# Optimization experiments

Measured on AMD Instinct MI355X. Metric: run time of the kernel, lower is better.

Reference implementation:

```python
import jax, jax.numpy as jnp
import numpy as np

C = 512
G = 32  # num_norm_groups
EPS = 1e-6


def setup_inputs() -> dict:
    key = jax.random.key(0)
    ks = jax.random.split(key, 10)
    B, H, W = 8, 64, 64
    s = 1.0 / np.sqrt(C)
    return {
        "x": jax.random.normal(ks[0], (B, C, H, W), dtype=jnp.float32),
        "gamma": jnp.ones((C,), jnp.float32),
        "beta": jnp.zeros((C,), jnp.float32),
        "Wq": jax.random.uniform(ks[1], (C, C), jnp.float32, -s, s),
        "bq": jax.random.uniform(ks[2], (C,), jnp.float32, -s, s),
        "Wk": jax.random.uniform(ks[3], (C, C), jnp.float32, -s, s),
        "bk": jax.random.uniform(ks[4], (C,), jnp.float32, -s, s),
        "Wv": jax.random.uniform(ks[5], (C, C), jnp.float32, -s, s),
        "bv": jax.random.uniform(ks[6], (C,), jnp.float32, -s, s),
        "Wo": jax.random.uniform(ks[7], (C, C), jnp.float32, -s, s),
    }


def group_norm(x, gamma, beta):
    # x: [B, C, H, W]; normalize over each group of C//G channels and all spatial dims
    B, Cc, H, W = x.shape
    xg = x.reshape(B, G, Cc // G, H, W)
    mean = jnp.mean(xg, axis=(2, 3, 4), keepdims=True)
    var = jnp.var(xg, axis=(2, 3, 4), keepdims=True)
    xg = (xg - mean) * jax.lax.rsqrt(var + EPS)
    x = xg.reshape(B, Cc, H, W)
    return x * gamma[None, :, None, None] + beta[None, :, None, None]


def reference(x, gamma, beta, Wq, bq, Wk, bk, Wv, bv, Wo):
    B, Cc, H, W = x.shape
    out = group_norm(x, gamma, beta)
    # [B, C, H, W] -> [B, H*W, C]
    out = out.transpose(0, 2, 3, 1).reshape(B, H * W, Cc)
    q = out @ Wq.T + bq
    k = out @ Wk.T + bk
    v = out @ Wv.T + bv
    score = jnp.einsum('bic,bjc->bij', q, k) / jnp.sqrt(jnp.float32(Cc))
    score = jax.nn.softmax(score, axis=-1)
    out = jnp.einsum('bij,bjc->bic', score, v)
    out = out @ Wo.T
    out = out.reshape(B, H, W, Cc).transpose(0, 3, 1, 2)
    return out + x
```

## Files before the change

kernel.cpp:

```cpp
#include <hip/hip_runtime.h>
#include <hip/hip_bf16.h>
#include <cstdint>
#include <cstddef>

typedef __hip_bfloat16 BF;
typedef __attribute__((ext_vector_type(8))) short bhalf8;
typedef __attribute__((ext_vector_type(4))) float floatx4;

#define NB 8
#define NC 512
#define NHW 4096
#define NG 32

__device__ __forceinline__ float b2f(short h) {
    union { unsigned u; float f; } c;
    c.u = ((unsigned)(unsigned short)h) << 16;
    return c.f;
}
__device__ __forceinline__ short f2b(float f) {
    __hip_bfloat16 h = __float2bfloat16(f);
    short s;
    __builtin_memcpy(&s, &h, 2);
    return s;
}

__device__ __forceinline__ void gload16(const BF* g, BF* l) {
    __builtin_amdgcn_global_load_lds(
        (const __attribute__((address_space(1))) void*)g,
        (__attribute__((address_space(3))) void*)l, 16, 0, 0);
}

__device__ __forceinline__ void BARRIER() {
    asm volatile("" ::: "memory");
    __builtin_amdgcn_s_barrier();
    asm volatile("" ::: "memory");
}
#define WAITVM(N) asm volatile("s_waitcnt vmcnt(" #N ")" ::: "memory")
#define WAITLGKM0() asm volatile("s_waitcnt lgkmcnt(0)" ::: "memory")
#define SB0() __builtin_amdgcn_sched_barrier(0)

#define DSR(dst, base, IMM) \
    asm volatile("ds_read_b128 %0, %1 offset:" #IMM : "=&v"(dst) : "v"(base))

__device__ __forceinline__ void xcd_swizzle(int& bx, int& by) {
    const int gx = gridDim.x;
    const int nwg = gx * gridDim.y;
    if ((nwg & 7) == 0) {
        const int lin = by * gx + bx;
        const int cpx = nwg >> 3;
        const int s = (lin & 7) * cpx + (lin >> 3);
        bx = s % gx;
        by = s / gx;
    }
}

struct QKVPtrs {
    BF* q; BF* k; BF* v;
    const float* bq; const float* bk; const float* bv;
};

__global__ __launch_bounds__(256) void f2b_convert4(const float* __restrict__ s0,
                                                    const float* __restrict__ s1,
                                                    const float* __restrict__ s2,
                                                    const float* __restrict__ s3,
                                                    BF* __restrict__ dst) {
    const int which = blockIdx.x >> 8;
    const float* src = (which == 0) ? s0 : (which == 1) ? s1 : (which == 2) ? s2 : s3;
    BF* d = dst + (long)which * (NC * NC);
    const int i = ((blockIdx.x & 255) * 256 + threadIdx.x) * 4;
    float4 v = *(const float4*)&src[i];
    d[i]     = __float2bfloat16(v.x);
    d[i + 1] = __float2bfloat16(v.y);
    d[i + 2] = __float2bfloat16(v.z);
    d[i + 3] = __float2bfloat16(v.w);
}

__global__ __launch_bounds__(256) void gn_stats_part(const float* __restrict__ x,
                                                     float2* __restrict__ part) {
    const int bg = blockIdx.x, qi = blockIdx.y;
    const long base = (long)bg * 65536 + (long)qi * 16384;
    float s = 0.f, q = 0.f;
    for (int i = threadIdx.x * 4; i < 16384; i += 256 * 4) {
        float4 v4 = *(const float4*)&x[base + i];
        s += v4.x + v4.y + v4.z + v4.w;
        q += v4.x * v4.x + v4.y * v4.y + v4.z * v4.z + v4.w * v4.w;
    }
#pragma unroll
    for (int o = 32; o; o >>= 1) { s += __shfl_down(s, o); q += __shfl_down(q, o); }
    __shared__ float rs[4], rq[4];
    const int w = threadIdx.x >> 6;
    if ((threadIdx.x & 63) == 0) { rs[w] = s; rq[w] = q; }
    __syncthreads();
    if (threadIdx.x == 0) {
        s = rs[0] + rs[1] + rs[2] + rs[3];
        q = rq[0] + rq[1] + rq[2] + rq[3];
        part[bg * 4 + qi] = make_float2(s, q);
    }
}

__global__ __launch_bounds__(256) void gn_finalize(const float2* __restrict__ part,
                                                   float* __restrict__ stats) {
    const int bg = threadIdx.x;
    float s = 0.f, q = 0.f;
#pragma unroll
    for (int j = 0; j < 4; j++) {
        float2 p = part[bg * 4 + j];
        s += p.x; q += p.y;
    }
    float mean = s * (1.f / 65536.f);
    float var = q * (1.f / 65536.f) - mean * mean;
    stats[2 * bg]     = mean;
    stats[2 * bg + 1] = rsqrtf(fmaxf(var, 0.f) + 1e-6f);
}

__global__ __launch_bounds__(256) void gn_apply(const float* __restrict__ x,
                                                const float* __restrict__ gamma,
                                                const float* __restrict__ beta,
                                                const float* __restrict__ stats,
                                                BF* __restrict__ n) {
    __shared__ float tile[64][65];
    const int b = blockIdx.z, c0 = blockIdx.y * 64, s0 = blockIdx.x * 64;
    const long xbase = ((long)b * NC + c0) * NHW + s0;
#pragma unroll
    for (int i = 0; i < 16; i++) {
        int lin = i * 256 + threadIdx.x;
        int cl = lin >> 6, sl = lin & 63;
        int c = c0 + cl;
        float2 mr = ((const float2*)stats)[b * NG + (c >> 4)];
        float v = x[xbase + (long)cl * NHW + sl];
        v = (v - mr.x) * mr.y * gamma[c] + beta[c];
        tile[cl][sl] = v;
    }
    __syncthreads();
    const long nbase = ((long)b * NHW + s0) * NC + c0;
#pragma unroll
    for (int i = 0; i < 16; i++) {
        int lin = i * 256 + threadIdx.x;
        int sl = lin >> 6, cl = lin & 63;
        n[nbase + (long)sl * NC + cl] = __float2bfloat16(tile[cl][sl]);
    }
}

#define RD_A_LO(b0, b1) { DSR(aR[0][0],b0,0);    DSR(aR[1][0],b0,2048); \
                          DSR(aR[2][0],b0,4096); DSR(aR[3][0],b0,6144); \
                          DSR(aR[0][1],b1,0);    DSR(aR[1][1],b1,2048); \
                          DSR(aR[2][1],b1,4096); DSR(aR[3][1],b1,6144); }
#define RD_A_HI(b0, b1) { DSR(aR[0][0],b0,8192);  DSR(aR[1][0],b0,10240); \
                          DSR(aR[2][0],b0,12288); DSR(aR[3][0],b0,14336); \
                          DSR(aR[0][1],b1,8192);  DSR(aR[1][1],b1,10240); \
                          DSR(aR[2][1],b1,12288); DSR(aR[3][1],b1,14336); }
#define RD_B_LO(b0, b1) { DSR(bR[0][0],b0,0);    DSR(bR[1][0],b0,2048); \
                          DSR(bR[0][1],b1,0);    DSR(bR[1][1],b1,2048); }
#define RD_B_HI(b0, b1) { DSR(bR[2][0],b0,4096); DSR(bR[3][0],b0,6144); \
                          DSR(bR[2][1],b1,4096); DSR(bR[3][1],b1,6144); }
#define QUAD(M0, N0)                                                                     \
    {                                                                                    \
        _Pragma("unroll") for (int ks = 0; ks < 2; ks++)                                 \
            _Pragma("unroll") for (int mf = (M0); mf < (M0) + 4; mf++)                   \
                _Pragma("unroll") for (int nf = (N0); nf < (N0) + 2; nf++)               \
                    acc[mf][nf] = __builtin_amdgcn_mfma_f32_16x16x32_bf16(               \
                        aR[mf & 3][ks], bR[nf][ks], acc[mf][nf], 0, 0, 0);               \
    }

template <bool BIAS, bool TRANS, bool RESID, bool QKV>
__global__ __launch_bounds__(512) void gemm256(
    const BF* __restrict__ A, long aStride,
    const BF* __restrict__ Bm, long bStride,
    BF* __restrict__ C, long cStride,
    const float* __restrict__ bias,
    const float* __restrict__ resid, float* __restrict__ outF,
    int M, int N, int K, float scale, long lda, long ldb, QKVPtrs P)
{
    __shared__ __align__(16) char sL[131072];
    const int tid = threadIdx.x;
    const int wave = tid >> 6, lane = tid & 63;
    int bxi = blockIdx.x, byi = blockIdx.y;
    xcd_swizzle(bxi, byi);
    const int bm = byi * 256, bn = bxi * 256;
    const int zz = blockIdx.z;
    const BF* Ab = A + (long)zz * aStride + (long)bm * lda;
    const BF* Bb = Bm + (long)zz * bStride + (long)bn * ldb;

    const int d0 = tid * 16, d1 = 8192 + tid * 16;
    const int r0 = d0 >> 7, r1 = d1 >> 7;
    const int c0s = ((d0 ^ ((r0 & 7) << 4)) & 127) >> 1;
    const int c1s = ((d1 ^ ((r1 & 7) << 4)) & 127) >> 1;
    const long sA0 = (long)r0 * lda + c0s, sA1 = (long)r1 * lda + c1s;
    const long sB0 = (long)r0 * ldb + c0s, sB1 = (long)r1 * ldb + c1s;
    const int lds0 = wave * 1024;
    const int lds1 = 8192 + wave * 1024;

    const int lr = lane & 15, lk2 = (lane >> 4) * 16;
    const int swz = (lr & 7) << 4;
    const int sb0 = lr * 128 + (lk2 ^ swz);
    const int sb1 = lr * 128 + ((lk2 + 64) ^ swz);
    const int aReg = (wave >> 2) * 16384;
    const int bReg = (2 + ((wave >> 1) & 1)) * 16384 + (wave & 1) * 8192;
    const int aI0 = aReg + sb0, aI1 = aReg + sb1;
    const int bI0 = bReg + sb0, bI1 = bReg + sb1;
    const int aJ0 = aI0 + 65536, aJ1 = aI1 + 65536;
    const int bJ0 = bI0 + 65536, bJ1 = bI1 + 65536;

    auto STAGE = [&](int t, int region, int dbuf) {
        const bool isA = region < 2;
        const long ld = isA ? lda : ldb;
        const BF* g = (isA ? (Ab + (long)region * 128 * ld)
                           : (Bb + (long)(region - 2) * 128 * ld)) + (long)t * 64;
        char* lb = sL + dbuf * 65536 + region * 16384;
        gload16(g + (isA ? sA0 : sB0), (BF*)(lb + lds0));
        gload16(g + (isA ? sA1 : sB1), (BF*)(lb + lds1));
    };

    floatx4 acc[8][4];
#pragma unroll
    for (int i = 0; i < 8; i++)
#pragma unroll
        for (int j = 0; j < 4; j++) acc[i][j] = (floatx4){0.f, 0.f, 0.f, 0.f};

    const int nt = K >> 6, ngrp = nt >> 1;

    STAGE(0, 0, 0); STAGE(0, 1, 0); STAGE(0, 2, 0); STAGE(0, 3, 0);
    WAITVM(4);
    STAGE(1, 2, 1); STAGE(1, 3, 1); STAGE(1, 0, 1);
    WAITVM(6);
    BARRIER();

    bhalf8 aR[4][2], bR[4][2];

    for (int g = 0; g < ngrp; ++g) {
        const bool st = (g < ngrp - 1);
        const int t2 = 2 * g + 2, t3 = 2 * g + 3;

        RD_A_LO(aI0, aI1);
        RD_B_LO(bI0, bI1);
        if (!(wave & 2)) { RD_B_HI(bI0, bI1); }
        STAGE(2 * g + 1, 1, 1);
        BARRIER(); WAITLGKM0(); SB0();
        __builtin_amdgcn_s_setprio(1);
        QUAD(0, 0);
        __builtin_amdgcn_s_setprio(0);
        BARRIER();

        if (wave & 2) { RD_B_HI(bI0, bI1); }
        if (st) STAGE(t2, 2, 0);
        BARRIER(); WAITLGKM0(); SB0();
        __builtin_amdgcn_s_setprio(1);
        QUAD(0, 2);
        __builtin_amdgcn_s_setprio(0);
        BARRIER();

        RD_A_HI(aI0, aI1);
        if (st) STAGE(t2, 3, 0);
        BARRIER(); WAITLGKM0(); SB0();
        __builtin_amdgcn_s_setprio(1);
        QUAD(4, 0);
        __builtin_amdgcn_s_setprio(0);
        BARRIER();

        if (st) STAGE(t2, 0, 0);
        BARRIER(); SB0();
        __builtin_amdgcn_s_setprio(1);
        QUAD(4, 2);
        __builtin_amdgcn_s_setprio(0);
        if (st) { WAITVM(6); } else { WAITVM(0); }
        BARRIER();

        RD_A_LO(aJ0, aJ1);
        RD_B_LO(bJ0, bJ1);
        if (!(wave & 2)) { RD_B_HI(bJ0, bJ1); }
        if (st) STAGE(t2, 1, 0);
        BARRIER(); WAITLGKM0(); SB0();
        __builtin_amdgcn_s_setprio(1);
        QUAD(0, 0);
        __builtin_amdgcn_s_setprio(0);
        BARRIER();

        if (wave & 2) { RD_B_HI(bJ0, bJ1); }
        if (st) STAGE(t3, 2, 1);
        BARRIER(); WAITLGKM0(); SB0();
        __builtin_amdgcn_s_setprio(1);
        QUAD(0, 2);
        __builtin_amdgcn_s_setprio(0);
        BARRIER();

        RD_A_HI(aJ0, aJ1);
        if (st) STAGE(t3, 3, 1);
        BARRIER(); WAITLGKM0(); SB0();
        __builtin_amdgcn_s_setprio(1);
        QUAD(4, 0);
        __builtin_amdgcn_s_setprio(0);
        BARRIER();

        if (st) STAGE(t3, 0, 1);
        BARRIER(); SB0();
        __builtin_amdgcn_s_setprio(1);
        QUAD(4, 2);
        __builtin_amdgcn_s_setprio(0);
        if (st) { WAITVM(6); }
        BARRIER();
    }

    const int wm = (wave >> 2) * 128, wn = (wave & 3) * 64;
    if (QKV) {
        const int sec = bn >> 9;
        const int cb = bn & 511;
        BF* Cb = (sec == 0 ? P.q : sec == 1 ? P.k : P.v) + (long)zz * cStride;
        const float* bb = (sec == 0 ? P.bq : sec == 1 ? P.bk : P.bv);
#pragma unroll
        for (int nf = 0; nf < 4; nf++) {
            const int col = cb + wn + nf * 16 + lr;
            const float bvv = bb[col];
#pragma unroll
            for (int mf = 0; mf < 8; mf++) {
                const int row0 = bm + wm + mf * 16 + (lane >> 4) * 4;
#pragma unroll
                for (int r = 0; r < 4; r++) {
                    float v = acc[mf][nf][r] * scale + bvv;
                    if (sec == 2) Cb[(long)col * M + row0 + r] = __float2bfloat16(v);
                    else          Cb[(long)(row0 + r) * NC + col] = __float2bfloat16(v);
                }
            }
        }
        return;
    }
    if (RESID) {
        float* Ob = outF + (long)zz * cStride;
        const float* Xb = resid + (long)zz * cStride;
#pragma unroll
        for (int nf = 0; nf < 4; nf++) {
            const int col = bn + wn + nf * 16 + lr;
#pragma unroll
            for (int mf = 0; mf < 8; mf++) {
                const int row0 = bm + wm + mf * 16 + (lane >> 4) * 4;
                const long a = (long)col * M + row0;
                float4 xv = *(const float4*)&Xb[a];
                float4 ov;
                ov.x = acc[mf][nf][0] * scale + xv.x;
                ov.y = acc[mf][nf][1] * scale + xv.y;
                ov.z = acc[mf][nf][2] * scale + xv.z;
                ov.w = acc[mf][nf][3] * scale + xv.w;
                *(float4*)&Ob[a] = ov;
            }
        }
        return;
    }
    BF* Cb = C + (long)zz * cStride;
#pragma unroll
    for (int nf = 0; nf < 4; nf++) {
        const int col = bn + wn + nf * 16 + lr;
        const float bv = BIAS ? bias[col] : 0.0f;
#pragma unroll
        for (int mf = 0; mf < 8; mf++) {
            const int row0 = bm + wm + mf * 16 + (lane >> 4) * 4;
#pragma unroll
            for (int r = 0; r < 4; r++) {
                float v = acc[mf][nf][r] * scale + bv;
                if (TRANS) Cb[(long)col * M + row0 + r] = __float2bfloat16(v);
                else       Cb[(long)(row0 + r) * N + col] = __float2bfloat16(v);
            }
        }
    }
}

template <bool BIAS, bool TRANS>
__global__ __launch_bounds__(256, 2) void gemm128(
    const BF* __restrict__ A, long aStride,
    const BF* __restrict__ Bm, long bStride,
    BF* __restrict__ C, long cStride,
    const float* __restrict__ bias,
    int M, int N, int K, float scale)
{
    __shared__ __align__(16) BF sA[128 * 32];
    __shared__ __align__(16) BF sB[128 * 32];
    const int tid = threadIdx.x;
    const int wave = tid >> 6, lane = tid & 63;
    int bxi = blockIdx.x, byi = blockIdx.y;
    xcd_swizzle(bxi, byi);
    const int bm = byi * 128, bn = bxi * 128;
    const BF* Ab = A + (long)blockIdx.z * aStride + (long)bm * K;
    const BF* Bb = Bm + (long)blockIdx.z * bStride + (long)bn * K;

    const int srow = wave * 32 + (lane >> 2);
    const int sk = (lane & 3) * 8;
    const BF* gA0 = Ab + (long)srow * K + sk;
    const BF* gA1 = gA0 + (long)16 * K;
    const BF* gB0 = Bb + (long)srow * K + sk;
    const BF* gB1 = gB0 + (long)16 * K;
    BF* lA0 = &sA[(wave * 32) * 32];
    BF* lA1 = &sA[(wave * 32 + 16) * 32];
    BF* lB0 = &sB[(wave * 32) * 32];
    BF* lB1 = &sB[(wave * 32 + 16) * 32];

    floatx4 acc[4][4];
#pragma unroll
    for (int i = 0; i < 4; i++)
#pragma unroll
        for (int j = 0; j < 4; j++) acc[i][j] = (floatx4){0.f, 0.f, 0.f, 0.f};

    const int wm = (wave >> 1) * 64, wn = (wave & 1) * 64;
    const int lr = lane & 15, lk = (lane >> 4) * 8;

    for (int k0 = 0; k0 < K; k0 += 32) {
        __syncthreads();
        gload16(gA0 + k0, lA0);
        gload16(gA1 + k0, lA1);
        gload16(gB0 + k0, lB0);
        gload16(gB1 + k0, lB1);
        __syncthreads();
        bhalf8 af[4], bfr[4];
#pragma unroll
        for (int i = 0; i < 4; i++)
            af[i] = *(const bhalf8*)&sA[(wm + i * 16 + lr) * 32 + lk];
#pragma unroll
        for (int i = 0; i < 4; i++)
            bfr[i] = *(const bhalf8*)&sB[(wn + i * 16 + lr) * 32 + lk];
#pragma unroll
        for (int mi = 0; mi < 4; mi++)
#pragma unroll
            for (int ni = 0; ni < 4; ni++)
                acc[mi][ni] = __builtin_amdgcn_mfma_f32_16x16x32_bf16(
                    af[mi], bfr[ni], acc[mi][ni], 0, 0, 0);
    }

    BF* Cb = C + (long)blockIdx.z * cStride;
#pragma unroll
    for (int ni = 0; ni < 4; ni++) {
        const int col = bn + wn + ni * 16 + lr;
        const float bv = BIAS ? bias[col] : 0.0f;
#pragma unroll
        for (int mi = 0; mi < 4; mi++) {
            const int row0 = bm + wm + mi * 16 + (lane >> 4) * 4;
#pragma unroll
            for (int r = 0; r < 4; r++) {
                float v = acc[mi][ni][r] * scale + bv;
                if (TRANS) Cb[(long)col * M + row0 + r] = __float2bfloat16(v);
                else       Cb[(long)(row0 + r) * N + col] = __float2bfloat16(v);
            }
        }
    }
}

__global__ __launch_bounds__(256, 2) void gemm64(
    const BF* __restrict__ A, long aStride,
    const BF* __restrict__ Bm, long bStride,
    BF* __restrict__ C, long cStride,
    int N, int K, float scale)
{
    __shared__ __align__(16) BF sA[64 * 32];
    __shared__ __align__(16) BF sB[128 * 32];
    const int tid = threadIdx.x;
    const int wave = tid >> 6, lane = tid & 63;
    int bxi = blockIdx.x, byi = blockIdx.y;
    xcd_swizzle(bxi, byi);
    const int bm = byi * 64, bn = bxi * 128;
    const BF* Ab = A + (long)blockIdx.z * aStride + (long)bm * K;
    const BF* Bb = Bm + (long)blockIdx.z * bStride + (long)bn * K;

    const int rowoff = lane >> 2, sk = (lane & 3) * 8;
    const BF* gA0 = Ab + (long)(wave * 16 + rowoff) * K + sk;
    const BF* gB0 = Bb + (long)(wave * 32 + rowoff) * K + sk;
    const BF* gB1 = gB0 + (long)16 * K;
    BF* lA0 = &sA[(wave * 16) * 32];
    BF* lB0 = &sB[(wave * 32) * 32];
    BF* lB1 = &sB[(wave * 32 + 16) * 32];

    floatx4 acc[2][4];
#pragma unroll
    for (int i = 0; i < 2; i++)
#pragma unroll
        for (int j = 0; j < 4; j++) acc[i][j] = (floatx4){0.f, 0.f, 0.f, 0.f};

    const int wm = (wave >> 1) * 32, wn = (wave & 1) * 64;
    const int lr = lane & 15, lk = (lane >> 4) * 8;

    for (int k0 = 0; k0 < K; k0 += 32) {
        __syncthreads();
        gload16(gA0 + k0, lA0);
        gload16(gB0 + k0, lB0);
        gload16(gB1 + k0, lB1);
        __syncthreads();
        bhalf8 af[2], bfr[4];
#pragma unroll
        for (int i = 0; i < 2; i++)
            af[i] = *(const bhalf8*)&sA[(wm + i * 16 + lr) * 32 + lk];
#pragma unroll
        for (int i = 0; i < 4; i++)
            bfr[i] = *(const bhalf8*)&sB[(wn + i * 16 + lr) * 32 + lk];
#pragma unroll
        for (int mi = 0; mi < 2; mi++)
#pragma unroll
            for (int ni = 0; ni < 4; ni++)
                acc[mi][ni] = __builtin_amdgcn_mfma_f32_16x16x32_bf16(
                    af[mi], bfr[ni], acc[mi][ni], 0, 0, 0);
    }

    BF* Cb = C + (long)blockIdx.z * cStride;
#pragma unroll
    for (int ni = 0; ni < 4; ni++) {
        const int col = bn + wn + ni * 16 + lr;
#pragma unroll
        for (int mi = 0; mi < 2; mi++) {
            const int row0 = bm + wm + mi * 16 + (lane >> 4) * 4;
#pragma unroll
            for (int r = 0; r < 4; r++)
                Cb[(long)(row0 + r) * N + col] = __float2bfloat16(acc[mi][ni][r] * scale);
        }
    }
}

__global__ __launch_bounds__(256) void softmax4096(BF* __restrict__ S) {
    const long base = (long)blockIdx.x * 4096 + threadIdx.x * 16;
    const int tid = threadIdx.x, w = tid >> 6;
    bhalf8 u = *(bhalf8*)&S[base];
    bhalf8 u2 = *(bhalf8*)&S[base + 8];
    float v[16];
    float m = -1e30f;
#pragma unroll
    for (int j = 0; j < 8; j++) { v[j] = b2f(u[j]); v[8 + j] = b2f(u2[j]); }
#pragma unroll
    for (int j = 0; j < 16; j++) m = fmaxf(m, v[j]);
#pragma unroll
    for (int o = 32; o; o >>= 1) m = fmaxf(m, __shfl_xor(m, o));
    __shared__ float rm[4], rs[4];
    if ((tid & 63) == 0) rm[w] = m;
    __syncthreads();
    m = fmaxf(fmaxf(rm[0], rm[1]), fmaxf(rm[2], rm[3]));
    float s = 0.f;
#pragma unroll
    for (int j = 0; j < 16; j++) { v[j] = __expf(v[j] - m); s += v[j]; }
#pragma unroll
    for (int o = 32; o; o >>= 1) s += __shfl_xor(s, o);
    if ((tid & 63) == 0) rs[w] = s;
    __syncthreads();
    s = rs[0] + rs[1] + rs[2] + rs[3];
    const float inv = 1.0f / s;
#pragma unroll
    for (int j = 0; j < 8; j++) { u[j] = f2b(v[j] * inv); u2[j] = f2b(v[8 + j] * inv); }
    *(bhalf8*)&S[base] = u;
    *(bhalf8*)&S[base + 8] = u2;
}

extern "C" void kernel_launch(void* const* d_in, const int* in_sizes, int n_in,
                              void* d_out, int out_size, void* d_ws, size_t ws_size,
                              hipStream_t stream) {
    const float* x     = (const float*)d_in[0];
    const float* gamma = (const float*)d_in[1];
    const float* beta  = (const float*)d_in[2];
    const float* Wq    = (const float*)d_in[3];
    const float* bq    = (const float*)d_in[4];
    const float* Wk    = (const float*)d_in[5];
    const float* bk    = (const float*)d_in[6];
    const float* Wv    = (const float*)d_in[7];
    const float* bv    = (const float*)d_in[8];
    const float* Wo    = (const float*)d_in[9];
    float* out = (float*)d_out;

    const long ACTB = (long)NHW * NC;
    const long SB   = (long)NHW * NHW;
    const long WSZ  = (long)NC * NC;

    char* ws = (char*)d_ws;
    float* stats = (float*)ws;
    float2* part = (float2*)(ws + 2048);
    BF* wb = (BF*)(ws + 16384);
    BF* q  = wb + 4 * WSZ;
    BF* kk = q + NB * ACTB;
    BF* vT = kk + NB * ACTB;
    BF* R  = vT + NB * ACTB;
    BF* n = R;
    BF* S = R;

    const size_t base_need = 16384ull + (size_t)4 * WSZ * 2 + (size_t)3 * NB * ACTB * 2;
    long sroom = (ws_size > base_need) ? (long)((ws_size - base_need) / (SB * 2)) : 1;
    int chunk = (int)(sroom < 1 ? 1 : (sroom > NB ? NB : sroom));
    while (NB % chunk) chunk--;

    QKVPtrs qkv = { q, kk, vT, bq, bk, bv };
    QKVPtrs nil = { nullptr, nullptr, nullptr, nullptr, nullptr, nullptr };

    f2b_convert4<<<1024, 256, 0, stream>>>(Wq, Wk, Wv, Wo, wb);

    gn_stats_part<<<dim3(NB * NG, 4), 256, 0, stream>>>(x, part);
    gn_finalize<<<1, 256, 0, stream>>>(part, stats);
    gn_apply<<<dim3(NHW / 64, NC / 64, NB), 256, 0, stream>>>(x, gamma, beta, stats, n);

    gemm256<false, false, false, true><<<dim3(1536 / 256, NHW / 256, NB), 512, 0, stream>>>(
        n, ACTB, wb, 0, nullptr, ACTB, nullptr, nullptr, nullptr,
        NHW, 1536, NC, 1.0f, NC, NC, qkv);

    const float iscl = 0.044194173824159216f;
    for (int b0 = 0; b0 < NB; b0 += chunk) {
        gemm256<false, false, false, false><<<dim3(NHW / 256, NHW / 256, chunk), 512, 0, stream>>>(
            q + b0 * ACTB, ACTB, kk + b0 * ACTB, ACTB, S, SB, nullptr, nullptr, nullptr,
            NHW, NHW, NC, iscl, NC, NC, nil);
        softmax4096<<<NHW * chunk, 256, 0, stream>>>(S);
        if (chunk >= 2)
            gemm128<false, false><<<dim3(NC / 128, NHW / 128, chunk), 256, 0, stream>>>(
                S, SB, vT + b0 * ACTB, ACTB, q + b0 * ACTB, ACTB, nullptr, NHW, NC, NHW, 1.0f);
        else
            gemm64<<<dim3(NC / 128, NHW / 64, chunk), 256, 0, stream>>>(
                S, SB, vT + b0 * ACTB, ACTB, q + b0 * ACTB, ACTB, NC, NHW, 1.0f);
    }

    gemm256<false, true, true, false><<<dim3(NC / 256, NHW / 256, NB), 512, 0, stream>>>(
        q, ACTB, wb + 3 * WSZ, 0, nullptr, ACTB, nullptr, x, out, NHW, NC, NC, 1.0f, NC, NC, nil);
}
```

Measured before the change: 836.6 us.

## Use split-K 256-tile GEMM for P@V with fp32 partials and a reduce kernel

The score-times-V GEMM now runs on the large 256x256 MFMA kernel, with K split in two across the z dimension so that enough workgroups are launched. Each half writes its fp32 partial result to workspace, and a new splitk_reduce kernel sums the two halves and converts them to bf16. The change also adds partial lgkmcnt waits and sched barriers after each MFMA quad, and folds the template flags into a single MODE parameter, dropping the unused bias and transpose paths and the gemm64 kernel. In exchange it adds fp32 partial traffic to and from workspace plus an extra kernel launch. The split path falls back to gemm128 when the workspace is too small or chunk is below 2.

```diff
diff --git a/kernel.cpp b/kernel.cpp
--- a/kernel.cpp
+++ b/kernel.cpp
@@ -37,6 +37,7 @@
 }
 #define WAITVM(N) asm volatile("s_waitcnt vmcnt(" #N ")" ::: "memory")
 #define WAITLGKM0() asm volatile("s_waitcnt lgkmcnt(0)" ::: "memory")
+#define WAITLGKM8() asm volatile("s_waitcnt lgkmcnt(8)" ::: "memory")
 #define SB0() __builtin_amdgcn_sched_barrier(0)
 
 #define DSR(dst, base, IMM) \
@@ -162,12 +163,11 @@
                         aR[mf & 3][ks], bR[nf][ks], acc[mf][nf], 0, 0, 0);               \
     }
 
-template <bool BIAS, bool TRANS, bool RESID, bool QKV>
+template <int MODE>
 __global__ __launch_bounds__(512) void gemm256(
     const BF* __restrict__ A, long aStride,
     const BF* __restrict__ Bm, long bStride,
     BF* __restrict__ C, long cStride,
-    const float* __restrict__ bias,
     const float* __restrict__ resid, float* __restrict__ outF,
     int M, int N, int K, float scale, long lda, long ldb, QKVPtrs P)
 {
@@ -178,8 +178,10 @@
     xcd_swizzle(bxi, byi);
     const int bm = byi * 256, bn = bxi * 256;
     const int zz = blockIdx.z;
-    const BF* Ab = A + (long)zz * aStride + (long)bm * lda;
-    const BF* Bb = Bm + (long)zz * bStride + (long)bn * ldb;
+    const int bz = (MODE == 3) ? (zz >> 1) : zz;
+    const int kh = (MODE == 3) ? (zz & 1) : 0;
+    const BF* Ab = A + (long)bz * aStride + (long)kh * K + (long)bm * lda;
+    const BF* Bb = Bm + (long)bz * bStride + (long)kh * K + (long)bn * ldb;
 
     const int d0 = tid * 16, d1 = 8192 + tid * 16;
     const int r0 = d0 >> 7, r1 = d1 >> 7;
@@ -235,9 +237,11 @@
         RD_B_LO(bI0, bI1);
         if (!(wave & 2)) { RD_B_HI(bI0, bI1); }
         STAGE(2 * g + 1, 1, 1);
+        WAITLGKM8();
         BARRIER(); WAITLGKM0(); SB0();
         __builtin_amdgcn_s_setprio(1);
         QUAD(0, 0);
+        SB0();
         __builtin_amdgcn_s_setprio(0);
         BARRIER();
 
@@ -246,6 +250,7 @@
         BARRIER(); WAITLGKM0(); SB0();
         __builtin_amdgcn_s_setprio(1);
         QUAD(0, 2);
+        SB0();
         __builtin_amdgcn_s_setprio(0);
         BARRIER();
 
@@ -254,6 +259,7 @@
         BARRIER(); WAITLGKM0(); SB0();
         __builtin_amdgcn_s_setprio(1);
         QUAD(4, 0);
+        SB0();
         __builtin_amdgcn_s_setprio(0);
         BARRIER();
 
@@ -261,6 +267,7 @@
         BARRIER(); SB0();
         __builtin_amdgcn_s_setprio(1);
         QUAD(4, 2);
+        SB0();
         __builtin_amdgcn_s_setprio(0);
         if (st) { WAITVM(6); } else { WAITVM(0); }
         BARRIER();
@@ -269,9 +276,11 @@
         RD_B_LO(bJ0, bJ1);
         if (!(wave & 2)) { RD_B_HI(bJ0, bJ1); }
         if (st) STAGE(t2, 1, 0);
+        WAITLGKM8();
         BARRIER(); WAITLGKM0(); SB0();
         __builtin_amdgcn_s_setprio(1);
         QUAD(0, 0);
+        SB0();
         __builtin_amdgcn_s_setprio(0);
         BARRIER();
 
@@ -280,6 +289,7 @@
         BARRIER(); WAITLGKM0(); SB0();
         __builtin_amdgcn_s_setprio(1);
         QUAD(0, 2);
+        SB0();
         __builtin_amdgcn_s_setprio(0);
         BARRIER();
 
@@ -288,6 +298,7 @@
         BARRIER(); WAITLGKM0(); SB0();
         __builtin_amdgcn_s_setprio(1);
         QUAD(4, 0);
+        SB0();
         __builtin_amdgcn_s_setprio(0);
         BARRIER();
 
@@ -295,13 +306,14 @@
         BARRIER(); SB0();
         __builtin_amdgcn_s_setprio(1);
         QUAD(4, 2);
+        SB0();
         __builtin_amdgcn_s_setprio(0);
         if (st) { WAITVM(6); }
         BARRIER();
     }
 
     const int wm = (wave >> 2) * 128, wn = (wave & 3) * 64;
-    if (QKV) {
+    if (MODE == 4) {
         const int sec = bn >> 9;
         const int cb = bn & 511;
         BF* Cb = (sec == 0 ? P.q : sec == 1 ? P.k : P.v) + (long)zz * cStride;
@@ -323,7 +335,22 @@
         }
         return;
     }
-    if (RESID) {
+    if (MODE == 3) {
+        float* Ob = outF + (long)zz * cStride;
+#pragma unroll
+        for (int nf = 0; nf < 4; nf++) {
+            const int col = bn + wn + nf * 16 + lr;
+#pragma unroll
+            for (int mf = 0; mf < 8; mf++) {
+                const int row0 = bm + wm + mf * 16 + (lane >> 4) * 4;
+#pragma unroll
+                for (int r = 0; r < 4; r++)
+                    Ob[(long)(row0 + r) * N + col] = acc[mf][nf][r] * scale;
+            }
+        }
+        return;
+    }
+    if (MODE == 2) {
         float* Ob = outF + (long)zz * cStride;
         const float* Xb = resid + (long)zz * cStride;
 #pragma unroll
@@ -348,18 +375,30 @@
 #pragma unroll
     for (int nf = 0; nf < 4; nf++) {
         const int col = bn + wn + nf * 16 + lr;
-        const float bv = BIAS ? bias[col] : 0.0f;
 #pragma unroll
         for (int mf = 0; mf < 8; mf++) {
             const int row0 = bm + wm + mf * 16 + (lane >> 4) * 4;
 #pragma unroll
-            for (int r = 0; r < 4; r++) {
-                float v = acc[mf][nf][r] * scale + bv;
-                if (TRANS) Cb[(long)col * M + row0 + r] = __float2bfloat16(v);
-                else       Cb[(long)(row0 + r) * N + col] = __float2bfloat16(v);
-            }
+            for (int r = 0; r < 4; r++)
+                Cb[(long)(row0 + r) * N + col] = __float2bfloat16(acc[mf][nf][r] * scale);
         }
     }
+}
+
+__global__ __launch_bounds__(256) void splitk_reduce(const float* __restrict__ P,
+                                                     BF* __restrict__ dst,
+                                                     long perBatch) {
+    const long off = ((long)blockIdx.x * 256 + threadIdx.x) * 4;
+    const float* p0 = P + (long)blockIdx.y * 2 * perBatch;
+    float4 a = *(const float4*)&p0[off];
+    float4 b = *(const float4*)&p0[perBatch + off];
+    BF* d = dst + (long)blockIdx.y * perBatch + off;
+    short4 o;
+    o.x = f2b(a.x + b.x);
+    o.y = f2b(a.y + b.y);
+    o.z = f2b(a.z + b.z);
+    o.w = f2b(a.w + b.w);
+    *(short4*)d = o;
 }
 
 template <bool BIAS, bool TRANS>
@@ -440,74 +479,6 @@
     }
 }
 
-__global__ __launch_bounds__(256, 2) void gemm64(
-    const BF* __restrict__ A, long aStride,
-    const BF* __restrict__ Bm, long bStride,
-    BF* __restrict__ C, long cStride,
-    int N, int K, float scale)
-{
-    __shared__ __align__(16) BF sA[64 * 32];
-    __shared__ __align__(16) BF sB[128 * 32];
-    const int tid = threadIdx.x;
-    const int wave = tid >> 6, lane = tid & 63;
-    int bxi = blockIdx.x, byi = blockIdx.y;
-    xcd_swizzle(bxi, byi);
-    const int bm = byi * 64, bn = bxi * 128;
-    const BF* Ab = A + (long)blockIdx.z * aStride + (long)bm * K;
-    const BF* Bb = Bm + (long)blockIdx.z * bStride + (long)bn * K;
-
-    const int rowoff = lane >> 2, sk = (lane & 3) * 8;
-    const BF* gA0 = Ab + (long)(wave * 16 + rowoff) * K + sk;
-    const BF* gB0 = Bb + (long)(wave * 32 + rowoff) * K + sk;
-    const BF* gB1 = gB0 + (long)16 * K;
-    BF* lA0 = &sA[(wave * 16) * 32];
-    BF* lB0 = &sB[(wave * 32) * 32];
-    BF* lB1 = &sB[(wave * 32 + 16) * 32];
-
-    floatx4 acc[2][4];
-#pragma unroll
-    for (int i = 0; i < 2; i++)
-#pragma unroll
-        for (int j = 0; j < 4; j++) acc[i][j] = (floatx4){0.f, 0.f, 0.f, 0.f};
-
-    const int wm = (wave >> 1) * 32, wn = (wave & 1) * 64;
-    const int lr = lane & 15, lk = (lane >> 4) * 8;
-
-    for (int k0 = 0; k0 < K; k0 += 32) {
-        __syncthreads();
-        gload16(gA0 + k0, lA0);
-        gload16(gB0 + k0, lB0);
-        gload16(gB1 + k0, lB1);
-        __syncthreads();
-        bhalf8 af[2], bfr[4];
-#pragma unroll
-        for (int i = 0; i < 2; i++)
-            af[i] = *(const bhalf8*)&sA[(wm + i * 16 + lr) * 32 + lk];
-#pragma unroll
-        for (int i = 0; i < 4; i++)
-            bfr[i] = *(const bhalf8*)&sB[(wn + i * 16 + lr) * 32 + lk];
-#pragma unroll
-        for (int mi = 0; mi < 2; mi++)
-#pragma unroll
-            for (int ni = 0; ni < 4; ni++)
-                acc[mi][ni] = __builtin_amdgcn_mfma_f32_16x16x32_bf16(
-                    af[mi], bfr[ni], acc[mi][ni], 0, 0, 0);
-    }
-
-    BF* Cb = C + (long)blockIdx.z * cStride;
-#pragma unroll
-    for (int ni = 0; ni < 4; ni++) {
-        const int col = bn + wn + ni * 16 + lr;
-#pragma unroll
-        for (int mi = 0; mi < 2; mi++) {
-            const int row0 = bm + wm + mi * 16 + (lane >> 4) * 4;
-#pragma unroll
-            for (int r = 0; r < 4; r++)
-                Cb[(long)(row0 + r) * N + col] = __float2bfloat16(acc[mi][ni][r] * scale);
-        }
-    }
-}
-
 __global__ __launch_bounds__(256) void softmax4096(BF* __restrict__ S) {
     const long base = (long)blockIdx.x * 4096 + threadIdx.x * 16;
     const int tid = threadIdx.x, w = tid >> 6;
@@ -575,6 +546,11 @@
     int chunk = (int)(sroom < 1 ? 1 : (sroom > NB ? NB : sroom));
     while (NB % chunk) chunk--;
 
+    float* Pf = (float*)(R + (long)chunk * SB);
+    const size_t splitNeed = base_need + (size_t)chunk * SB * 2
+                           + (size_t)chunk * 2 * ACTB * 4;
+    const bool doSplit = (chunk >= 2) && (ws_size >= splitNeed);
+
     QKVPtrs qkv = { q, kk, vT, bq, bk, bv };
     QKVPtrs nil = { nullptr, nullptr, nullptr, nullptr, nullptr, nullptr };
 
@@ -584,24 +560,28 @@
     gn_finalize<<<1, 256, 0, stream>>>(part, stats);
     gn_apply<<<dim3(NHW / 64, NC / 64, NB), 256, 0, stream>>>(x, gamma, beta, stats, n);
 
-    gemm256<false, false, false, true><<<dim3(1536 / 256, NHW / 256, NB), 512, 0, stream>>>(
-        n, ACTB, wb, 0, nullptr, ACTB, nullptr, nullptr, nullptr,
+    gemm256<4><<<dim3(1536 / 256, NHW / 256, NB), 512, 0, stream>>>(
+        n, ACTB, wb, 0, nullptr, ACTB, nullptr, nullptr,
         NHW, 1536, NC, 1.0f, NC, NC, qkv);
 
     const float iscl = 0.044194173824159216f;
     for (int b0 = 0; b0 < NB; b0 += chunk) {
-        gemm256<false, false, false, false><<<dim3(NHW / 256, NHW / 256, chunk), 512, 0, stream>>>(
-            q + b0 * ACTB, ACTB, kk + b0 * ACTB, ACTB, S, SB, nullptr, nullptr, nullptr,
+        gemm256<0><<<dim3(NHW / 256, NHW / 256, chunk), 512, 0, stream>>>(
+            q + b0 * ACTB, ACTB, kk + b0 * ACTB, ACTB, S, SB, nullptr, nullptr,
             NHW, NHW, NC, iscl, NC, NC, nil);
         softmax4096<<<NHW * chunk, 256, 0, stream>>>(S);
-        if (chunk >= 2)
+        if (doSplit) {
+            gemm256<3><<<dim3(NC / 256, NHW / 256, chunk * 2), 512, 0, stream>>>(
+                S, SB, vT + b0 * ACTB, ACTB, nullptr, ACTB, nullptr, Pf,
+                NHW, NC, NHW / 2, 1.0f, NHW, NHW, nil);
+            splitk_reduce<<<dim3((unsigned)(ACTB / 1024), chunk), 256, 0, stream>>>(
+                Pf, q + b0 * ACTB, ACTB);
+        } else {
             gemm128<false, false><<<dim3(NC / 128, NHW / 128, chunk), 256, 0, stream>>>(
                 S, SB, vT + b0 * ACTB, ACTB, q + b0 * ACTB, ACTB, nullptr, NHW, NC, NHW, 1.0f);
-        else
-            gemm64<<<dim3(NC / 128, NHW / 64, chunk), 256, 0, stream>>>(
-                S, SB, vT + b0 * ACTB, ACTB, q + b0 * ACTB, ACTB, NC, NHW, 1.0f);
-    }
-
-    gemm256<false, true, true, false><<<dim3(NC / 256, NHW / 256, NB), 512, 0, stream>>>(
-        q, ACTB, wb + 3 * WSZ, 0, nullptr, ACTB, nullptr, x, out, NHW, NC, NC, 1.0f, NC, NC, nil);
-}
+        }
+    }
+
+    gemm256<2><<<dim3(NC / 256, NHW / 256, NB), 512, 0, stream>>>(
+        q, ACTB, wb + 3 * WSZ, 0, nullptr, ACTB, x, out, NHW, NC, NC, 1.0f, NC, NC, nil);
+}
```

Result: no change. 833.6 us (-0.4%).
